# Optimization experiments

Hardware: AMD Instinct MI355X
Metric: run time of the kernel (lower is better)

The kernel has to match this reference:

```python
import jax, jax.numpy as jnp
import numpy as np

B = 2048
INPUT_SIZE = 40960
HIDDEN = 256
ACTIVE = 30  # ~active features per chess position


def _multi_hot(key):
    idx = jax.random.randint(key, (B, ACTIVE), 0, INPUT_SIZE)
    oh = jnp.zeros((B, INPUT_SIZE), jnp.float32)
    return oh.at[jnp.arange(B)[:, None], idx].set(1.0)


def setup_inputs() -> dict:
    key = jax.random.key(0)
    kw, kb, ks, k1, k2, k3, k4 = jax.random.split(key, 7)
    white_onehot = _multi_hot(kw)
    black_onehot = _multi_hot(kb)
    stm = jax.random.randint(ks, (B, 1), 0, 2).astype(jnp.float32)
    # parameters (PyTorch Linear layout: weight [out, in])
    ft_w = jax.random.normal(k1, (HIDDEN, INPUT_SIZE), jnp.float32) * 0.02
    ft_b = jnp.zeros((HIDDEN,), jnp.float32)
    l1_w = jax.random.normal(k2, (32, HIDDEN * 2), jnp.float32) * 0.05
    l1_b = jnp.zeros((32,), jnp.float32)
    l2_w = jax.random.normal(k3, (32, 32), jnp.float32) * 0.1
    l2_b = jnp.zeros((32,), jnp.float32)
    l3_w = jax.random.normal(k4, (1, 32), jnp.float32) * 0.1
    l3_b = jnp.zeros((1,), jnp.float32)
    return dict(white_onehot=white_onehot, black_onehot=black_onehot, stm=stm,
                ft_w=ft_w, ft_b=ft_b, l1_w=l1_w, l1_b=l1_b,
                l2_w=l2_w, l2_b=l2_b, l3_w=l3_w, l3_b=l3_b)


def reference(white_onehot, black_onehot, stm,
              ft_w, ft_b, l1_w, l1_b, l2_w, l2_b, l3_w, l3_b):
    # feature transformer applied to dense one-hots (the wasteful dense GEMM)
    wh = jnp.clip(white_onehot @ ft_w.T + ft_b, 0.0, 1.0)  # [B, H]
    bh = jnp.clip(black_onehot @ ft_w.T + ft_b, 0.0, 1.0)  # [B, H]
    # side-to-move dependent perspective ordering
    hidden = jnp.where(stm.astype(bool),
                       jnp.concatenate([wh, bh], axis=-1),
                       jnp.concatenate([bh, wh], axis=-1))  # [B, 2H]
    x = jnp.clip(hidden @ l1_w.T + l1_b, 0.0, 1.0)
    x = jnp.clip(x @ l2_w.T + l2_b, 0.0, 1.0)
    return x @ l3_w.T + l3_b  # [B, 1]
```

## Files before the change

kernel.cpp:

```cpp
#include <hip/hip_runtime.h>

#define BATCH 2048
#define IN_SZ 40960
#define HID 256
#define MAXF 48

__global__ __launch_bounds__(256) void ft_transpose(const float* __restrict__ ftw,
                                                    float* __restrict__ ftT) {
    __shared__ float tile[32][33];
    const int tx = threadIdx.x;
    const int ty = threadIdx.y;
    const int bx = blockIdx.x;
    const int by = blockIdx.y;

    const int col = bx * 32 + tx;
#pragma unroll
    for (int j = 0; j < 32; j += 8) {
        const int row = by * 32 + ty + j;
        tile[ty + j][tx] = ftw[(size_t)row * IN_SZ + col];
    }
    __syncthreads();

    const int ocol = by * 32 + tx;
#pragma unroll
    for (int j = 0; j < 32; j += 8) {
        const int orow = bx * 32 + ty + j;
        ftT[(size_t)orow * HID + ocol] = tile[tx][ty + j];
    }
}

template <bool TRANSPOSED>
__global__ __launch_bounds__(256) void nnue_fused(
    const float* __restrict__ wo, const float* __restrict__ bo,
    const float* __restrict__ stm,
    const float* __restrict__ ftw,
    const float* __restrict__ ftb,
    const float* __restrict__ l1w, const float* __restrict__ l1b,
    const float* __restrict__ l2w, const float* __restrict__ l2b,
    const float* __restrict__ l3w, const float* __restrict__ l3b,
    float* __restrict__ out) {
    __shared__ int   idxw[MAXF], idxb[MAXF];
    __shared__ int   cntw, cntb;
    __shared__ float hidden[2 * HID];
    __shared__ float x1[32], x2[32];

    const int b = blockIdx.x;
    const int t = threadIdx.x;

    if (t == 0) { cntw = 0; cntb = 0; }
    __syncthreads();

    const float4* wrow = (const float4*)(wo + (size_t)b * IN_SZ);
    const float4* brow = (const float4*)(bo + (size_t)b * IN_SZ);
    for (int i = t; i < IN_SZ / 4; i += 256) {
        float4 v = wrow[i];
        float4 u = brow[i];
        if (v.x != 0.f) { int p = atomicAdd(&cntw, 1); idxw[p] = 4 * i + 0; }
        if (v.y != 0.f) { int p = atomicAdd(&cntw, 1); idxw[p] = 4 * i + 1; }
        if (v.z != 0.f) { int p = atomicAdd(&cntw, 1); idxw[p] = 4 * i + 2; }
        if (v.w != 0.f) { int p = atomicAdd(&cntw, 1); idxw[p] = 4 * i + 3; }
        if (u.x != 0.f) { int p = atomicAdd(&cntb, 1); idxb[p] = 4 * i + 0; }
        if (u.y != 0.f) { int p = atomicAdd(&cntb, 1); idxb[p] = 4 * i + 1; }
        if (u.z != 0.f) { int p = atomicAdd(&cntb, 1); idxb[p] = 4 * i + 2; }
        if (u.w != 0.f) { int p = atomicAdd(&cntb, 1); idxb[p] = 4 * i + 3; }
    }
    __syncthreads();

    const int h = t;
    float accw = ftb[h];
    float accb = accw;
    const int cw = cntw, cb = cntb;
    for (int j = 0; j < cw; ++j) {
        const int f = idxw[j];
        accw += TRANSPOSED ? ftw[(size_t)f * HID + h] : ftw[(size_t)h * IN_SZ + f];
    }
    for (int j = 0; j < cb; ++j) {
        const int f = idxb[j];
        accb += TRANSPOSED ? ftw[(size_t)f * HID + h] : ftw[(size_t)h * IN_SZ + f];
    }
    accw = fminf(fmaxf(accw, 0.f), 1.f);
    accb = fminf(fmaxf(accb, 0.f), 1.f);

    const bool s = (stm[b] != 0.f);
    hidden[h]       = s ? accw : accb;
    hidden[HID + h] = s ? accb : accw;
    __syncthreads();

    {
        const int o = t >> 3;
        const int part = t & 7;
        const float* w1 = l1w + o * (2 * HID);
        float sum = 0.f;
#pragma unroll 8
        for (int i = part; i < 2 * HID; i += 8)
            sum += hidden[i] * w1[i];
        sum += __shfl_xor(sum, 1);
        sum += __shfl_xor(sum, 2);
        sum += __shfl_xor(sum, 4);
        if (part == 0) x1[o] = fminf(fmaxf(sum + l1b[o], 0.f), 1.f);
    }
    __syncthreads();

    if (t < 32) {
        const float* w2 = l2w + t * 32;
        float sum = l2b[t];
#pragma unroll
        for (int i = 0; i < 32; ++i) sum += x1[i] * w2[i];
        x2[t] = fminf(fmaxf(sum, 0.f), 1.f);
    }
    __syncthreads();

    if (t == 0) {
        float sum = l3b[0];
#pragma unroll
        for (int i = 0; i < 32; ++i) sum += x2[i] * l3w[i];
        out[b] = sum;
    }
}

extern "C" void kernel_launch(void* const* d_in, const int* in_sizes, int n_in,
                              void* d_out, int out_size, void* d_ws, size_t ws_size,
                              hipStream_t stream) {
    const float* wo  = (const float*)d_in[0];
    const float* bo  = (const float*)d_in[1];
    const float* stm = (const float*)d_in[2];
    const float* ftw = (const float*)d_in[3];
    const float* ftb = (const float*)d_in[4];
    const float* l1w = (const float*)d_in[5];
    const float* l1b = (const float*)d_in[6];
    const float* l2w = (const float*)d_in[7];
    const float* l2b = (const float*)d_in[8];
    const float* l3w = (const float*)d_in[9];
    const float* l3b = (const float*)d_in[10];
    float* out = (float*)d_out;

    const size_t need = (size_t)IN_SZ * HID * sizeof(float);
    if (ws_size >= need) {
        float* ftT = (float*)d_ws;
        ft_transpose<<<dim3(IN_SZ / 32, HID / 32), dim3(32, 8), 0, stream>>>(ftw, ftT);
        nnue_fused<true><<<BATCH, 256, 0, stream>>>(wo, bo, stm, ftT, ftb,
                                                    l1w, l1b, l2w, l2b, l3w, l3b, out);
    } else {
        nnue_fused<false><<<BATCH, 256, 0, stream>>>(wo, bo, stm, ftw, ftb,
                                                     l1w, l1b, l2w, l2b, l3w, l3b, out);
    }
}
```

Before: 689.9 us.

## Split one-hot scan into grid-stride extract kernel feeding gather-MLP kernel

Moves the nonzero-index extraction out of the per-batch fused kernel into a separate grid-stride kernel over the whole one-hot matrices. It writes per-row counts and index lists to workspace via global atomics, and a second kernel gathers transposed feature-transformer rows and runs the MLP. It also skips per-element checks when a float4 sums to zero. The intent is better memory-bandwidth use for the dominant 670MB scan, at the cost of an extra memset, a kernel launch and global atomics.

```diff
diff --git a/kernel.cpp b/kernel.cpp
--- a/kernel.cpp
+++ b/kernel.cpp
@@ -2,8 +2,9 @@
 
 #define BATCH 2048
 #define IN_SZ 40960
-#define HID 256
-#define MAXF 48
+#define IN4   (IN_SZ / 4)
+#define HID   256
+#define LCAP  64
 
 __global__ __launch_bounds__(256) void ft_transpose(const float* __restrict__ ftw,
                                                     float* __restrict__ ftT) {
@@ -29,61 +30,60 @@
     }
 }
 
-template <bool TRANSPOSED>
-__global__ __launch_bounds__(256) void nnue_fused(
-    const float* __restrict__ wo, const float* __restrict__ bo,
+__global__ __launch_bounds__(256) void extract(const float* __restrict__ wo,
+                                               const float* __restrict__ bo,
+                                               int* __restrict__ cnt,
+                                               int* __restrict__ lists)
+{
+    const int persp = blockIdx.y;
+    const float4* __restrict__ src = (const float4*)(persp ? bo : wo);
+    const int stride = gridDim.x * blockDim.x;
+    for (int i = blockIdx.x * blockDim.x + threadIdx.x; i < BATCH * IN4; i += stride) {
+        const float4 v = src[i];
+        if (((v.x + v.y) + (v.z + v.w)) != 0.f) {
+            const int row = i / IN4;
+            const int f0  = (i - row * IN4) * 4;
+            int* c = cnt + row * 2 + persp;
+            int* l = lists + (row * 2 + persp) * LCAP;
+            if (v.x != 0.f) l[atomicAdd(c, 1)] = f0;
+            if (v.y != 0.f) l[atomicAdd(c, 1)] = f0 + 1;
+            if (v.z != 0.f) l[atomicAdd(c, 1)] = f0 + 2;
+            if (v.w != 0.f) l[atomicAdd(c, 1)] = f0 + 3;
+        }
+    }
+}
+
+__global__ __launch_bounds__(256) void ft_mlp(
+    const int* __restrict__ cnt, const int* __restrict__ lists,
     const float* __restrict__ stm,
-    const float* __restrict__ ftw,
-    const float* __restrict__ ftb,
+    const float* __restrict__ ftT, const float* __restrict__ ftb,
     const float* __restrict__ l1w, const float* __restrict__ l1b,
     const float* __restrict__ l2w, const float* __restrict__ l2b,
     const float* __restrict__ l3w, const float* __restrict__ l3b,
     float* __restrict__ out) {
-    __shared__ int   idxw[MAXF], idxb[MAXF];
-    __shared__ int   cntw, cntb;
+    __shared__ int   sidx[2 * LCAP];
     __shared__ float hidden[2 * HID];
     __shared__ float x1[32], x2[32];
 
     const int b = blockIdx.x;
     const int t = threadIdx.x;
 
-    if (t == 0) { cntw = 0; cntb = 0; }
-    __syncthreads();
-
-    const float4* wrow = (const float4*)(wo + (size_t)b * IN_SZ);
-    const float4* brow = (const float4*)(bo + (size_t)b * IN_SZ);
-    for (int i = t; i < IN_SZ / 4; i += 256) {
-        float4 v = wrow[i];
-        float4 u = brow[i];
-        if (v.x != 0.f) { int p = atomicAdd(&cntw, 1); idxw[p] = 4 * i + 0; }
-        if (v.y != 0.f) { int p = atomicAdd(&cntw, 1); idxw[p] = 4 * i + 1; }
-        if (v.z != 0.f) { int p = atomicAdd(&cntw, 1); idxw[p] = 4 * i + 2; }
-        if (v.w != 0.f) { int p = atomicAdd(&cntw, 1); idxw[p] = 4 * i + 3; }
-        if (u.x != 0.f) { int p = atomicAdd(&cntb, 1); idxb[p] = 4 * i + 0; }
-        if (u.y != 0.f) { int p = atomicAdd(&cntb, 1); idxb[p] = 4 * i + 1; }
-        if (u.z != 0.f) { int p = atomicAdd(&cntb, 1); idxb[p] = 4 * i + 2; }
-        if (u.w != 0.f) { int p = atomicAdd(&cntb, 1); idxb[p] = 4 * i + 3; }
-    }
-    __syncthreads();
-
-    const int h = t;
-    float accw = ftb[h];
+    if (t < 2 * LCAP) sidx[t] = lists[b * 2 * LCAP + t];
+    __syncthreads();
+
+    const int cw = cnt[b * 2 + 0];
+    const int cb = cnt[b * 2 + 1];
+
+    float accw = ftb[t];
     float accb = accw;
-    const int cw = cntw, cb = cntb;
-    for (int j = 0; j < cw; ++j) {
-        const int f = idxw[j];
-        accw += TRANSPOSED ? ftw[(size_t)f * HID + h] : ftw[(size_t)h * IN_SZ + f];
-    }
-    for (int j = 0; j < cb; ++j) {
-        const int f = idxb[j];
-        accb += TRANSPOSED ? ftw[(size_t)f * HID + h] : ftw[(size_t)h * IN_SZ + f];
-    }
+    for (int j = 0; j < cw; ++j) accw += ftT[(size_t)sidx[j] * HID + t];
+    for (int j = 0; j < cb; ++j) accb += ftT[(size_t)sidx[LCAP + j] * HID + t];
     accw = fminf(fmaxf(accw, 0.f), 1.f);
     accb = fminf(fmaxf(accb, 0.f), 1.f);
 
     const bool s = (stm[b] != 0.f);
-    hidden[h]       = s ? accw : accb;
-    hidden[HID + h] = s ? accb : accw;
+    hidden[t]       = s ? accw : accb;
+    hidden[HID + t] = s ? accb : accw;
     __syncthreads();
 
     {
@@ -113,6 +113,79 @@
     if (t == 0) {
         float sum = l3b[0];
 #pragma unroll
+        for (int i = 0; i < 32; ++i) sum += x2[i] * l3w[i];
+        out[b] = sum;
+    }
+}
+
+__global__ __launch_bounds__(256) void nnue_fused_fallback(
+    const float* __restrict__ wo, const float* __restrict__ bo,
+    const float* __restrict__ stm,
+    const float* __restrict__ ftw, const float* __restrict__ ftb,
+    const float* __restrict__ l1w, const float* __restrict__ l1b,
+    const float* __restrict__ l2w, const float* __restrict__ l2b,
+    const float* __restrict__ l3w, const float* __restrict__ l3b,
+    float* __restrict__ out) {
+    __shared__ int   idxw[LCAP], idxb[LCAP];
+    __shared__ int   cntw, cntb;
+    __shared__ float hidden[2 * HID];
+    __shared__ float x1[32], x2[32];
+
+    const int b = blockIdx.x;
+    const int t = threadIdx.x;
+    if (t == 0) { cntw = 0; cntb = 0; }
+    __syncthreads();
+
+    const float4* wrow = (const float4*)(wo + (size_t)b * IN_SZ);
+    const float4* brow = (const float4*)(bo + (size_t)b * IN_SZ);
+    for (int i = t; i < IN4; i += 256) {
+        float4 v = wrow[i];
+        float4 u = brow[i];
+        if (((v.x + v.y) + (v.z + v.w)) != 0.f) {
+            if (v.x != 0.f) idxw[atomicAdd(&cntw, 1)] = 4 * i;
+            if (v.y != 0.f) idxw[atomicAdd(&cntw, 1)] = 4 * i + 1;
+            if (v.z != 0.f) idxw[atomicAdd(&cntw, 1)] = 4 * i + 2;
+            if (v.w != 0.f) idxw[atomicAdd(&cntw, 1)] = 4 * i + 3;
+        }
+        if (((u.x + u.y) + (u.z + u.w)) != 0.f) {
+            if (u.x != 0.f) idxb[atomicAdd(&cntb, 1)] = 4 * i;
+            if (u.y != 0.f) idxb[atomicAdd(&cntb, 1)] = 4 * i + 1;
+            if (u.z != 0.f) idxb[atomicAdd(&cntb, 1)] = 4 * i + 2;
+            if (u.w != 0.f) idxb[atomicAdd(&cntb, 1)] = 4 * i + 3;
+        }
+    }
+    __syncthreads();
+
+    float accw = ftb[t], accb = accw;
+    for (int j = 0; j < cntw; ++j) accw += ftw[(size_t)t * IN_SZ + idxw[j]];
+    for (int j = 0; j < cntb; ++j) accb += ftw[(size_t)t * IN_SZ + idxb[j]];
+    accw = fminf(fmaxf(accw, 0.f), 1.f);
+    accb = fminf(fmaxf(accb, 0.f), 1.f);
+
+    const bool s = (stm[b] != 0.f);
+    hidden[t]       = s ? accw : accb;
+    hidden[HID + t] = s ? accb : accw;
+    __syncthreads();
+
+    {
+        const int o = t >> 3, part = t & 7;
+        const float* w1 = l1w + o * (2 * HID);
+        float sum = 0.f;
+        for (int i = part; i < 2 * HID; i += 8) sum += hidden[i] * w1[i];
+        sum += __shfl_xor(sum, 1);
+        sum += __shfl_xor(sum, 2);
+        sum += __shfl_xor(sum, 4);
+        if (part == 0) x1[o] = fminf(fmaxf(sum + l1b[o], 0.f), 1.f);
+    }
+    __syncthreads();
+    if (t < 32) {
+        float sum = l2b[t];
+        for (int i = 0; i < 32; ++i) sum += x1[i] * l2w[t * 32 + i];
+        x2[t] = fminf(fmaxf(sum, 0.f), 1.f);
+    }
+    __syncthreads();
+    if (t == 0) {
+        float sum = l3b[0];
         for (int i = 0; i < 32; ++i) sum += x2[i] * l3w[i];
         out[b] = sum;
     }
@@ -134,14 +207,25 @@
     const float* l3b = (const float*)d_in[10];
     float* out = (float*)d_out;
 
-    const size_t need = (size_t)IN_SZ * HID * sizeof(float);
-    if (ws_size >= need) {
-        float* ftT = (float*)d_ws;
+    const size_t ftT_bytes  = (size_t)IN_SZ * HID * sizeof(float);
+    const size_t cnt_off    = 44 * 1024 * 1024;
+    const size_t cnt_bytes  = (size_t)BATCH * 2 * sizeof(int);
+    const size_t list_off   = cnt_off + cnt_bytes;
+    const size_t list_bytes = (size_t)BATCH * 2 * LCAP * sizeof(int);
+    const size_t need       = list_off + list_bytes;
+
+    if (ws_size >= need && ftT_bytes <= cnt_off) {
+        float* ftT  = (float*)d_ws;
+        int* cnt    = (int*)((char*)d_ws + cnt_off);
+        int* lists  = (int*)((char*)d_ws + list_off);
+
+        hipMemsetAsync(cnt, 0, cnt_bytes, stream);
         ft_transpose<<<dim3(IN_SZ / 32, HID / 32), dim3(32, 8), 0, stream>>>(ftw, ftT);
-        nnue_fused<true><<<BATCH, 256, 0, stream>>>(wo, bo, stm, ftT, ftb,
-                                                    l1w, l1b, l2w, l2b, l3w, l3b, out);
+        extract<<<dim3(1024, 2), 256, 0, stream>>>(wo, bo, cnt, lists);
+        ft_mlp<<<BATCH, 256, 0, stream>>>(cnt, lists, stm, ftT, ftb,
+                                          l1w, l1b, l2w, l2b, l3w, l3b, out);
     } else {
-        nnue_fused<false><<<BATCH, 256, 0, stream>>>(wo, bo, stm, ftw, ftb,
-                                                     l1w, l1b, l2w, l2b, l3w, l3b, out);
-    }
-}
+        nnue_fused_fallback<<<BATCH, 256, 0, stream>>>(wo, bo, stm, ftw, ftb,
+                                                       l1w, l1b, l2w, l2b, l3w, l3b, out);
+    }
+}
```

Result: no change. 702.1 us (+1.8%).
